# Kernel optimization log

Hardware: AMD Instinct MI355X
Metric: run time of the kernel (lower is better)

The kernel has to match this reference:

```python
import jax, jax.numpy as jnp
import numpy as np

TEMPERATURE = 0.07
MASK_VAL = -9e15
EPS = 1e-8

def setup_inputs() -> dict:
    key = jax.random.key(0)
    features = jax.random.normal(key, (8192, 256), dtype=jnp.float32)
    return {"features": features}

def reference(features):
    # features: [N, D]
    N = features.shape[0]
    norm = jnp.linalg.norm(features, axis=-1, keepdims=True)
    f = features / jnp.maximum(norm, EPS)
    # cosine similarity via GEMM: [N, N]
    sim = f @ f.T
    idx = jnp.arange(N)
    # mask self-similarity BEFORE temperature scaling (as in the torch code)
    sim = jnp.where(idx[:, None] == idx[None, :], MASK_VAL, sim)
    sim = sim / TEMPERATURE
    # positive of row i is column (i - N//2) mod N (eye rolled by N//2 along dim 0)
    pos_col = (idx - N // 2) % N
    pos = sim[idx, pos_col]
    nll = -pos + jax.nn.logsumexp(sim, axis=-1)
    return nll.mean()
```

## Files before the change

### kernel.cpp

```cpp
#include <hip/hip_runtime.h>
#include <hip/hip_bf16.h>
#include <math.h>

#define N_ROWS 8192
#define D_DIM  256
#define HALF_N 4096
#define INV_T      14.285714285714286f
#define SCALE_LOG2 20.609929155556620f
#define NEG_SCALE  -20.609929155556620f
#define EPSV   1e-8f

typedef __attribute__((ext_vector_type(8))) short bf16x8;
typedef __attribute__((ext_vector_type(4))) float f32x4;

#define AS1 __attribute__((address_space(1)))
#define AS3 __attribute__((address_space(3)))

__device__ inline unsigned short f2bf(float x) {
    unsigned int u = __float_as_uint(x);
    unsigned int r = (u + 0x7fffu + ((u >> 16) & 1u)) >> 16;
    return (unsigned short)r;
}

__global__ __launch_bounds__(256) void k_norm(const float* __restrict__ feat,
                                              unsigned short* __restrict__ fbf,
                                              float* __restrict__ sumexp,
                                              float* __restrict__ out) {
    const int tid = threadIdx.x;
    const int gid = blockIdx.x * 256 + tid;
    if (gid < N_ROWS) sumexp[gid] = 0.f;
    if (gid == 0) out[0] = 0.f;

    const int w = tid >> 6, lane = tid & 63;
    const int row = blockIdx.x * 4 + w;
    const float4 v = ((const float4*)(feat + row * D_DIM))[lane];
    float ss = v.x*v.x + v.y*v.y + v.z*v.z + v.w*v.w;
    #pragma unroll
    for (int off = 32; off; off >>= 1) ss += __shfl_xor(ss, off);
    const float scale = 1.f / fmaxf(sqrtf(ss), EPSV);
    ushort4 o;
    o.x = f2bf(v.x * scale);
    o.y = f2bf(v.y * scale);
    o.z = f2bf(v.z * scale);
    o.w = f2bf(v.w * scale);
    ((ushort4*)(fbf + row * D_DIM))[lane] = o;
}

__global__ __launch_bounds__(256, 2) void k_sim(const unsigned short* __restrict__ fbf,
                                                float* __restrict__ sumexp) {
    __shared__ __align__(16) char Bs[32768];
    const int tid  = threadIdx.x;
    const int lane = tid & 63;
    const int w    = tid >> 6;
    const int q    = lane >> 4, l15 = lane & 15;
    const int rt = blockIdx.x >> 5, cs = blockIdx.x & 31;
    const int rowBase = rt * 128 + w * 32;

    {
        const char* Bg = (const char*)(fbf + (cs * 256) * D_DIM);
        #pragma unroll
        for (int i = 0; i < 8; ++i) {
            const int idx = i * 256 + tid;
            const int col = idx >> 5;
            const int cir = idx & 31;
            __builtin_amdgcn_global_load_lds(
                (const AS1 void*)(Bg + col * 512 + ((cir ^ (col & 7)) << 4)),
                (AS3 void*)(Bs + idx * 16), 16, 0, 0);
        }
    }

    bf16x8 afrag[8][2];
    #pragma unroll
    for (int t = 0; t < 8; ++t)
        #pragma unroll
        for (int ri = 0; ri < 2; ++ri)
            afrag[t][ri] = *(const bf16x8*)(fbf + (rowBase + ri*16 + l15) * D_DIM
                                                + t*32 + q*8);

    float rsum[2][4];
    #pragma unroll
    for (int ri = 0; ri < 2; ++ri)
        #pragma unroll
        for (int r = 0; r < 4; ++r) rsum[ri][r] = 0.f;

    #pragma unroll 1
    for (int jt = 0; jt < 4; ++jt) {
        const int colBase = cs * 256 + jt * 64;

        __syncthreads();

        f32x4 acc[2][4];
        #pragma unroll
        for (int ri = 0; ri < 2; ++ri)
            #pragma unroll
            for (int ci = 0; ci < 4; ++ci) acc[ri][ci] = (f32x4){0.f, 0.f, 0.f, 0.f};

        #pragma unroll
        for (int t = 0; t < 8; ++t) {
            bf16x8 bfrag[4];
            #pragma unroll
            for (int ci = 0; ci < 4; ++ci) {
                const int c   = ci * 16 + l15;
                const int cir = t * 4 + q;
                bfrag[ci] = *(const bf16x8*)(Bs + c * 512 + ((cir ^ (c & 7)) << 4));
            }
            #pragma unroll
            for (int ri = 0; ri < 2; ++ri)
                #pragma unroll
                for (int ci = 0; ci < 4; ++ci)
                    acc[ri][ci] = __builtin_amdgcn_mfma_f32_16x16x32_bf16(
                        afrag[t][ri], bfrag[ci], acc[ri][ci], 0, 0, 0);
        }

        if (jt < 3) {
            __syncthreads();
            const char* Bg = (const char*)(fbf + (colBase + 64) * D_DIM);
            #pragma unroll
            for (int i = 0; i < 8; ++i) {
                const int idx = i * 256 + tid;
                const int col = idx >> 5;
                const int cir = idx & 31;
                __builtin_amdgcn_global_load_lds(
                    (const AS1 void*)(Bg + col * 512 + ((cir ^ (col & 7)) << 4)),
                    (AS3 void*)(Bs + idx * 16), 16, 0, 0);
            }
        }

        #pragma unroll
        for (int ri = 0; ri < 2; ++ri) {
            const int trow = rowBase + ri * 16;
            #pragma unroll
            for (int ci = 0; ci < 4; ++ci) {
                const int tcol = colBase + ci * 16;
                if (trow == tcol) {
                    #pragma unroll
                    for (int r = 0; r < 4; ++r) {
                        const float e = __builtin_amdgcn_exp2f(
                            __builtin_fmaf(acc[ri][ci][r], SCALE_LOG2, NEG_SCALE));
                        rsum[ri][r] += (q * 4 + r == l15) ? 0.f : e;
                    }
                } else {
                    #pragma unroll
                    for (int r = 0; r < 4; ++r)
                        rsum[ri][r] += __builtin_amdgcn_exp2f(
                            __builtin_fmaf(acc[ri][ci][r], SCALE_LOG2, NEG_SCALE));
                }
            }
        }
    }

    #pragma unroll
    for (int ri = 0; ri < 2; ++ri)
        #pragma unroll
        for (int r = 0; r < 4; ++r) {
            float s = rsum[ri][r];
            s += __shfl_xor(s, 1);
            s += __shfl_xor(s, 2);
            s += __shfl_xor(s, 4);
            s += __shfl_xor(s, 8);
            if (l15 == 0)
                atomicAdd(&sumexp[rowBase + ri * 16 + q * 4 + r], s);
        }
}

__global__ __launch_bounds__(256) void k_nll(const float* __restrict__ feat,
                                             const float* __restrict__ sumexp,
                                             float* __restrict__ out) {
    __shared__ float red[4];
    const int tid = threadIdx.x, w = tid >> 6, lane = tid & 63;
    const int i  = blockIdx.x * 4 + w;
    const int pc = (i + HALF_N) & (N_ROWS - 1);
    const float4 a = ((const float4*)(feat + i  * D_DIM))[lane];
    const float4 b = ((const float4*)(feat + pc * D_DIM))[lane];
    float dab = a.x*b.x + a.y*b.y + a.z*b.z + a.w*b.w;
    float daa = a.x*a.x + a.y*a.y + a.z*a.z + a.w*a.w;
    float dbb = b.x*b.x + b.y*b.y + b.z*b.z + b.w*b.w;
    #pragma unroll
    for (int off = 32; off; off >>= 1) {
        dab += __shfl_xor(dab, off);
        daa += __shfl_xor(daa, off);
        dbb += __shfl_xor(dbb, off);
    }
    if (lane == 0) {
        const float pos = dab / (fmaxf(sqrtf(daa), EPSV) * fmaxf(sqrtf(dbb), EPSV));
        red[w] = INV_T + logf(sumexp[i]) - pos * INV_T;
    }
    __syncthreads();
    if (tid == 0)
        atomicAdd(out, (red[0] + red[1] + red[2] + red[3]) * (1.f / N_ROWS));
}

extern "C" void kernel_launch(void* const* d_in, const int* in_sizes, int n_in,
                              void* d_out, int out_size, void* d_ws, size_t ws_size,
                              hipStream_t stream) {
    const float* feat = (const float*)d_in[0];
    char* ws = (char*)d_ws;
    unsigned short* fbf = (unsigned short*)ws;
    float* sumexp = (float*)(ws + 4u * 1024u * 1024u);

    k_norm<<<N_ROWS / 4, 256, 0, stream>>>(feat, fbf, sumexp, (float*)d_out);
    k_sim <<<2048,       256, 0, stream>>>(fbf, sumexp);
    k_nll <<<N_ROWS / 4, 256, 0, stream>>>(feat, sumexp, (float*)d_out);
}
```

Measured before the change: 131.4 us.

## Restructure similarity tiling, fold positive dot into norm, fuse final reduction

```diff
diff --git a/kernel.cpp b/kernel.cpp
--- a/kernel.cpp
+++ b/kernel.cpp
@@ -9,6 +9,7 @@
 #define SCALE_LOG2 20.609929155556620f
 #define NEG_SCALE  -20.609929155556620f
 #define EPSV   1e-8f
+#define GRID_SIM 512
 
 typedef __attribute__((ext_vector_type(8))) short bf16x8;
 typedef __attribute__((ext_vector_type(4))) float f32x4;
@@ -25,18 +26,28 @@
 __global__ __launch_bounds__(256) void k_norm(const float* __restrict__ feat,
                                               unsigned short* __restrict__ fbf,
                                               float* __restrict__ sumexp,
+                                              float* __restrict__ pos,
+                                              unsigned int* __restrict__ counter,
                                               float* __restrict__ out) {
     const int tid = threadIdx.x;
     const int gid = blockIdx.x * 256 + tid;
     if (gid < N_ROWS) sumexp[gid] = 0.f;
-    if (gid == 0) out[0] = 0.f;
+    if (gid == 0) { out[0] = 0.f; *counter = 0u; }
 
     const int w = tid >> 6, lane = tid & 63;
     const int row = blockIdx.x * 4 + w;
+    const int pc  = (row + HALF_N) & (N_ROWS - 1);
     const float4 v = ((const float4*)(feat + row * D_DIM))[lane];
-    float ss = v.x*v.x + v.y*v.y + v.z*v.z + v.w*v.w;
-    #pragma unroll
-    for (int off = 32; off; off >>= 1) ss += __shfl_xor(ss, off);
+    const float4 p = ((const float4*)(feat + pc  * D_DIM))[lane];
+    float ss  = v.x*v.x + v.y*v.y + v.z*v.z + v.w*v.w;
+    float sp  = p.x*p.x + p.y*p.y + p.z*p.z + p.w*p.w;
+    float dot = v.x*p.x + v.y*p.y + v.z*p.z + v.w*p.w;
+    #pragma unroll
+    for (int off = 32; off; off >>= 1) {
+        ss  += __shfl_xor(ss,  off);
+        sp  += __shfl_xor(sp,  off);
+        dot += __shfl_xor(dot, off);
+    }
     const float scale = 1.f / fmaxf(sqrtf(ss), EPSV);
     ushort4 o;
     o.x = f2bf(v.x * scale);
@@ -44,22 +55,30 @@
     o.z = f2bf(v.z * scale);
     o.w = f2bf(v.w * scale);
     ((ushort4*)(fbf + row * D_DIM))[lane] = o;
+    if (lane == 0)
+        pos[row] = dot / (fmaxf(sqrtf(ss), EPSV) * fmaxf(sqrtf(sp), EPSV));
 }
 
 __global__ __launch_bounds__(256, 2) void k_sim(const unsigned short* __restrict__ fbf,
-                                                float* __restrict__ sumexp) {
-    __shared__ __align__(16) char Bs[32768];
+                                                float* __restrict__ sumexp,
+                                                const float* __restrict__ pos,
+                                                unsigned int* __restrict__ counter,
+                                                float* __restrict__ out) {
+    __shared__ __align__(16) char Bs[65536];
+    __shared__ float redbuf[4];
+    __shared__ int isLast;
     const int tid  = threadIdx.x;
     const int lane = tid & 63;
     const int w    = tid >> 6;
     const int q    = lane >> 4, l15 = lane & 15;
-    const int rt = blockIdx.x >> 5, cs = blockIdx.x & 31;
-    const int rowBase = rt * 128 + w * 32;
+    const int rt = blockIdx.x >> 2, cs = blockIdx.x & 3;
+    const int rowBase = rt * 64;
+    const int csBase  = cs * 2048;
 
     {
-        const char* Bg = (const char*)(fbf + (cs * 256) * D_DIM);
-        #pragma unroll
-        for (int i = 0; i < 8; ++i) {
+        const char* Bg = (const char*)fbf + (size_t)csBase * 512;
+        #pragma unroll
+        for (int i = 0; i < 16; ++i) {
             const int idx = i * 256 + tid;
             const int col = idx >> 5;
             const int cir = idx & 31;
@@ -69,54 +88,54 @@
         }
     }
 
-    bf16x8 afrag[8][2];
+    bf16x8 afrag[8][4];
     #pragma unroll
     for (int t = 0; t < 8; ++t)
         #pragma unroll
-        for (int ri = 0; ri < 2; ++ri)
+        for (int ri = 0; ri < 4; ++ri)
             afrag[t][ri] = *(const bf16x8*)(fbf + (rowBase + ri*16 + l15) * D_DIM
                                                 + t*32 + q*8);
 
-    float rsum[2][4];
-    #pragma unroll
-    for (int ri = 0; ri < 2; ++ri)
+    float rsum[4][4];
+    #pragma unroll
+    for (int ri = 0; ri < 4; ++ri)
         #pragma unroll
         for (int r = 0; r < 4; ++r) rsum[ri][r] = 0.f;
 
     #pragma unroll 1
-    for (int jt = 0; jt < 4; ++jt) {
-        const int colBase = cs * 256 + jt * 64;
+    for (int jt = 0; jt < 16; ++jt) {
+        const int colBase = csBase + jt * 128;
 
         __syncthreads();
 
-        f32x4 acc[2][4];
-        #pragma unroll
-        for (int ri = 0; ri < 2; ++ri)
-            #pragma unroll
-            for (int ci = 0; ci < 4; ++ci) acc[ri][ci] = (f32x4){0.f, 0.f, 0.f, 0.f};
+        f32x4 acc[4][2];
+        #pragma unroll
+        for (int ri = 0; ri < 4; ++ri)
+            #pragma unroll
+            for (int ci = 0; ci < 2; ++ci) acc[ri][ci] = (f32x4){0.f, 0.f, 0.f, 0.f};
 
         #pragma unroll
         for (int t = 0; t < 8; ++t) {
-            bf16x8 bfrag[4];
-            #pragma unroll
-            for (int ci = 0; ci < 4; ++ci) {
-                const int c   = ci * 16 + l15;
+            bf16x8 bfrag[2];
+            #pragma unroll
+            for (int ci = 0; ci < 2; ++ci) {
+                const int c   = w * 32 + ci * 16 + l15;
                 const int cir = t * 4 + q;
                 bfrag[ci] = *(const bf16x8*)(Bs + c * 512 + ((cir ^ (c & 7)) << 4));
             }
             #pragma unroll
-            for (int ri = 0; ri < 2; ++ri)
+            for (int ri = 0; ri < 4; ++ri)
                 #pragma unroll
-                for (int ci = 0; ci < 4; ++ci)
+                for (int ci = 0; ci < 2; ++ci)
                     acc[ri][ci] = __builtin_amdgcn_mfma_f32_16x16x32_bf16(
                         afrag[t][ri], bfrag[ci], acc[ri][ci], 0, 0, 0);
         }
 
-        if (jt < 3) {
+        if (jt < 15) {
             __syncthreads();
-            const char* Bg = (const char*)(fbf + (colBase + 64) * D_DIM);
-            #pragma unroll
-            for (int i = 0; i < 8; ++i) {
+            const char* Bg = (const char*)fbf + (size_t)(colBase + 128) * 512;
+            #pragma unroll
+            for (int i = 0; i < 16; ++i) {
                 const int idx = i * 256 + tid;
                 const int col = idx >> 5;
                 const int cir = idx & 31;
@@ -127,11 +146,11 @@
         }
 
         #pragma unroll
-        for (int ri = 0; ri < 2; ++ri) {
+        for (int ri = 0; ri < 4; ++ri) {
             const int trow = rowBase + ri * 16;
             #pragma unroll
-            for (int ci = 0; ci < 4; ++ci) {
-                const int tcol = colBase + ci * 16;
+            for (int ci = 0; ci < 2; ++ci) {
+                const int tcol = colBase + w * 32 + ci * 16;
                 if (trow == tcol) {
                     #pragma unroll
                     for (int r = 0; r < 4; ++r) {
@@ -150,7 +169,7 @@
     }
 
     #pragma unroll
-    for (int ri = 0; ri < 2; ++ri)
+    for (int ri = 0; ri < 4; ++ri)
         #pragma unroll
         for (int r = 0; r < 4; ++r) {
             float s = rsum[ri][r];
@@ -161,33 +180,29 @@
             if (l15 == 0)
                 atomicAdd(&sumexp[rowBase + ri * 16 + q * 4 + r], s);
         }
-}
-
-__global__ __launch_bounds__(256) void k_nll(const float* __restrict__ feat,
-                                             const float* __restrict__ sumexp,
-                                             float* __restrict__ out) {
-    __shared__ float red[4];
-    const int tid = threadIdx.x, w = tid >> 6, lane = tid & 63;
-    const int i  = blockIdx.x * 4 + w;
-    const int pc = (i + HALF_N) & (N_ROWS - 1);
-    const float4 a = ((const float4*)(feat + i  * D_DIM))[lane];
-    const float4 b = ((const float4*)(feat + pc * D_DIM))[lane];
-    float dab = a.x*b.x + a.y*b.y + a.z*b.z + a.w*b.w;
-    float daa = a.x*a.x + a.y*a.y + a.z*a.z + a.w*a.w;
-    float dbb = b.x*b.x + b.y*b.y + b.z*b.z + b.w*b.w;
-    #pragma unroll
-    for (int off = 32; off; off >>= 1) {
-        dab += __shfl_xor(dab, off);
-        daa += __shfl_xor(daa, off);
-        dbb += __shfl_xor(dbb, off);
-    }
-    if (lane == 0) {
-        const float pos = dab / (fmaxf(sqrtf(daa), EPSV) * fmaxf(sqrtf(dbb), EPSV));
-        red[w] = INV_T + logf(sumexp[i]) - pos * INV_T;
+
+    __threadfence();
+    if (tid == 0) {
+        unsigned int prev = __hip_atomic_fetch_add(counter, 1u, __ATOMIC_ACQ_REL,
+                                                   __HIP_MEMORY_SCOPE_AGENT);
+        isLast = (prev == GRID_SIM - 1);
     }
     __syncthreads();
-    if (tid == 0)
-        atomicAdd(out, (red[0] + red[1] + red[2] + red[3]) * (1.f / N_ROWS));
+    if (isLast) {
+        float accn = 0.f;
+        for (int i = tid; i < N_ROWS; i += 256) {
+            const float se = __hip_atomic_load(&sumexp[i], __ATOMIC_RELAXED,
+                                               __HIP_MEMORY_SCOPE_AGENT);
+            accn += logf(se) - pos[i] * INV_T;
+        }
+        #pragma unroll
+        for (int off = 32; off; off >>= 1) accn += __shfl_xor(accn, off);
+        if (lane == 0) redbuf[w] = accn;
+        __syncthreads();
+        if (tid == 0)
+            out[0] = INV_T + (redbuf[0] + redbuf[1] + redbuf[2] + redbuf[3])
+                             * (1.f / N_ROWS);
+    }
 }
 
 extern "C" void kernel_launch(void* const* d_in, const int* in_sizes, int n_in,
@@ -196,9 +211,12 @@
     const float* feat = (const float*)d_in[0];
     char* ws = (char*)d_ws;
     unsigned short* fbf = (unsigned short*)ws;
-    float* sumexp = (float*)(ws + 4u * 1024u * 1024u);
-
-    k_norm<<<N_ROWS / 4, 256, 0, stream>>>(feat, fbf, sumexp, (float*)d_out);
-    k_sim <<<2048,       256, 0, stream>>>(fbf, sumexp);
-    k_nll <<<N_ROWS / 4, 256, 0, stream>>>(feat, sumexp, (float*)d_out);
-}
+    float* sumexp = (float*)(ws + 4u*1024u*1024u);
+    float* pos    = (float*)(ws + 4u*1024u*1024u + 32u*1024u);
+    unsigned int* counter = (unsigned int*)(ws + 4u*1024u*1024u + 64u*1024u);
+
+    k_norm<<<N_ROWS / 4, 256, 0, stream>>>(feat, fbf, sumexp, pos, counter,
+                                           (float*)d_out);
+    k_sim <<<GRID_SIM,   256, 0, stream>>>(fbf, sumexp, pos, counter,
+                                           (float*)d_out);
+}
```

Measured after the change: 142.7 us. 8.6% more time.
